# Kernel optimization log

Measured on AMD Instinct MI355X. Metric: run time of the kernel, lower is better.

The kernel has to match this reference:

```python
import jax, jax.numpy as jnp
import numpy as np

NUM_GRAPHS = 512
LEAKY_SLOPE = 0.01


def _gconv(x, src, dst, w, W_root, W_rel, b_rel):
    # PyG GraphConv: out = lin_rel(sum_j w_ij * x_j) + lin_root(x)
    msg = x[src] * w[:, None]                       # [E, d] gather + scale
    agg = jax.ops.segment_sum(msg, dst, num_segments=x.shape[0])  # scatter-add
    return agg @ W_rel + b_rel + x @ W_root


def setup_inputs() -> dict:
    key = jax.random.key(0)
    ks = jax.random.split(key, 12)
    N, E, D, H, C = 100000, 1250000, 64, 64, 8
    x_embeddings = jax.random.normal(ks[0], (N, D), dtype=jnp.float32)
    edge_index = jax.random.randint(ks[1], (2, E), 0, N, dtype=jnp.int64)
    weights = jax.random.uniform(ks[2], (E,), dtype=jnp.float32)
    batch = jnp.sort(jax.random.randint(ks[3], (N,), 0, NUM_GRAPHS, dtype=jnp.int64))
    s1 = 1.0 / np.sqrt(D)
    s2 = 1.0 / np.sqrt(H)
    W1_root = jax.random.uniform(ks[4], (D, H), jnp.float32, -s1, s1)
    W1_rel = jax.random.uniform(ks[5], (D, H), jnp.float32, -s1, s1)
    b1 = jax.random.uniform(ks[6], (H,), jnp.float32, -s1, s1)
    W2_root = jax.random.uniform(ks[7], (H, H), jnp.float32, -s2, s2)
    W2_rel = jax.random.uniform(ks[8], (H, H), jnp.float32, -s2, s2)
    b2 = jax.random.uniform(ks[9], (H,), jnp.float32, -s2, s2)
    Wl_root = jax.random.uniform(ks[10], (H, C), jnp.float32, -s2, s2)
    bl = jax.random.uniform(ks[11], (C,), jnp.float32, -s2, s2)
    return {"x_embeddings": x_embeddings, "edge_index": edge_index,
            "weights": weights, "batch": batch,
            "W1_root": W1_root, "W1_rel": W1_rel, "b1": b1,
            "W2_root": W2_root, "W2_rel": W2_rel, "b2": b2,
            "Wl_root": Wl_root, "bl": bl}


def reference(x_embeddings, edge_index, weights, batch,
              W1_root, W1_rel, b1, W2_root, W2_rel, b2, Wl_root, bl):
    src, dst = edge_index[0], edge_index[1]
    x = _gconv(x_embeddings, src, dst, weights, W1_root, W1_rel, b1)
    x = jax.nn.leaky_relu(x, LEAKY_SLOPE)
    x = _gconv(x, src, dst, weights, W2_root, W2_rel, b2)
    x = jax.nn.leaky_relu(x, LEAKY_SLOPE)
    # global_mean_pool over graph ids
    summed = jax.ops.segment_sum(x, batch, num_segments=NUM_GRAPHS)
    counts = jax.ops.segment_sum(jnp.ones((x.shape[0],), x.dtype), batch,
                                 num_segments=NUM_GRAPHS)
    pooled = summed / jnp.maximum(counts, 1.0)[:, None]
    # final GraphConv applied with no edges: agg = 0 -> W_root x + b_rel
    out = pooled @ Wl_root + bl
    return out
```

## Files before the change

kernel.cpp:

```cpp
#include <hip/hip_runtime.h>

#define LEAKY_SLOPE 0.01f
#define NUM_GRAPHS 512
#define TILE 4096
#define NB_MAX 512
#define POOL_SPAN 8

typedef __attribute__((ext_vector_type(8))) short short8;
typedef __attribute__((ext_vector_type(4))) float f32x4;

static __device__ __forceinline__ unsigned short f2bf(float f) {
    unsigned u = __float_as_uint(f);
    u += 0x7FFFu + ((u >> 16) & 1u);
    return (unsigned short)(u >> 16);
}
static __device__ __forceinline__ float bf2f(unsigned short h) {
    return __uint_as_float(((unsigned)h) << 16);
}

static __device__ __forceinline__ int wave_incl_scan(int v, int lane) {
#pragma unroll
    for (int off = 1; off < 64; off <<= 1) {
        int t = __shfl_up(v, off, 64);
        if (lane >= off) v += t;
    }
    return v;
}

__global__ __launch_bounds__(256)
void mega_prep(const int* __restrict__ dst, int* __restrict__ bucketCnt, int E,
               int NB, int histBlocks,
               const float* __restrict__ x, unsigned short* __restrict__ xB,
               int xElems , int xBlocks,
               const float* __restrict__ W1rel, const float* __restrict__ W1root,
               const float* __restrict__ W2rel, const float* __restrict__ W2root,
               unsigned short* __restrict__ Bt1, unsigned short* __restrict__ Bt2) {
    const int bid = blockIdx.x;
    if (bid < histBlocks) {
        __shared__ int h[NB_MAX];
        for (int t = threadIdx.x; t < NB_MAX; t += 256) h[t] = 0;
        __syncthreads();
        const int base = bid * TILE;
#pragma unroll
        for (int i = 0; i < TILE / 256; ++i) {
            int e = base + i * 256 + threadIdx.x;
            if (e < E) atomicAdd(&h[dst[e] >> 8], 1);
        }
        __syncthreads();
        for (int t = threadIdx.x; t < NB; t += 256)
            if (h[t]) atomicAdd(&bucketCnt[t], h[t]);
    } else if (bid < histBlocks + xBlocks) {
        int i = (bid - histBlocks) * 256 + threadIdx.x;
        if (i < xElems) {
            float4 f = ((const float4*)x)[i];
            ushort4 o = make_ushort4(f2bf(f.x), f2bf(f.y), f2bf(f.z), f2bf(f.w));
            ((ushort4*)xB)[i] = o;
        }
    } else {
        int b2 = bid - histBlocks - xBlocks;
        for (int idx = b2 * 2048 + threadIdx.x; idx < (b2 + 1) * 2048; idx += 256) {
            int which = idx >> 13;
            int j = idx & 8191;
            int n = j >> 7, k = j & 127;
            const float* Wr = which ? W2rel : W1rel;
            const float* Wo = which ? W2root : W1root;
            float v = (k < 64) ? Wr[k * 64 + n] : Wo[(k - 64) * 64 + n];
            (which ? Bt2 : Bt1)[j] = f2bf(v);
        }
    }
}

__global__ __launch_bounds__(512)
void bscan_kernel(const int* __restrict__ bucketCnt, int* __restrict__ bucketBase,
                  int* __restrict__ cursor, int* __restrict__ rowStart,
                  float* __restrict__ pooled, int N, int E, int NB) {
    __shared__ int ws[8];
    const int t = threadIdx.x, lane = t & 63, wid = t >> 6;
    int v = (t < NB) ? bucketCnt[t] : 0;
    int s = wave_incl_scan(v, lane);
    if (lane == 63) ws[wid] = s;
    __syncthreads();
    int add = 0;
    for (int i = 0; i < wid; ++i) add += ws[i];
    if (t < NB) {
        int excl = s + add - v;
        bucketBase[t] = excl;
        cursor[t] = excl;
    }
    if (t == 0) rowStart[N] = E;
    float4 z = make_float4(0.f, 0.f, 0.f, 0.f);
#pragma unroll
    for (int i = 0; i < 16; ++i)
        ((float4*)pooled)[t * 16 + i] = z;
}

__global__ __launch_bounds__(256)
void p1b_partition(const int* __restrict__ src, const int* __restrict__ dst,
                   const float* __restrict__ w, int* __restrict__ cursor,
                   int2* __restrict__ tmp, int E, int NB) {
    __shared__ int h[NB_MAX];
    __shared__ int cur[NB_MAX];
    __shared__ int lstart[NB_MAX];
    __shared__ int gbase[NB_MAX];
    __shared__ int ws[4];
    __shared__ int2 pay[TILE];
    __shared__ unsigned short bk[TILE];

    for (int t = threadIdx.x; t < NB_MAX; t += 256) h[t] = 0;
    __syncthreads();

    const int base = blockIdx.x * TILE;
    int   myb[TILE / 256];
    int   myp[TILE / 256];
    float myw[TILE / 256];
#pragma unroll
    for (int i = 0; i < TILE / 256; ++i) {
        int e = base + i * 256 + threadIdx.x;
        if (e < E) {
            int d = dst[e];
            myb[i] = d >> 8;
            myp[i] = src[e] | ((d & 255) << 20);
            myw[i] = w[e];
            atomicAdd(&h[myb[i]], 1);
        } else {
            myb[i] = -1;
        }
    }
    __syncthreads();

    {
        const int t = threadIdx.x, lane = t & 63, wid = t >> 6;
        int a = h[2 * t], b = h[2 * t + 1];
        int s = wave_incl_scan(a + b, lane);
        if (lane == 63) ws[wid] = s;
        __syncthreads();
        int add = 0;
        for (int i = 0; i < wid; ++i) add += ws[i];
        int excl = s + add - (a + b);
        lstart[2 * t] = excl;
        lstart[2 * t + 1] = excl + a;
        cur[2 * t] = excl;
        cur[2 * t + 1] = excl + a;
    }
    __syncthreads();

#pragma unroll
    for (int i = 0; i < TILE / 256; ++i) {
        if (myb[i] >= 0) {
            int p = atomicAdd(&cur[myb[i]], 1);
            pay[p] = make_int2(myp[i], __float_as_int(myw[i]));
            bk[p] = (unsigned short)myb[i];
        }
    }
    __syncthreads();

    for (int t = threadIdx.x; t < NB; t += 256) {
        int c = h[t];
        if (c) gbase[t] = atomicAdd(&cursor[t], c);
    }
    __syncthreads();

    const int total = min(TILE, E - base);
    for (int s2 = threadIdx.x; s2 < total; s2 += 256) {
        int b2 = bk[s2];
        tmp[gbase[b2] + s2 - lstart[b2]] = pay[s2];
    }
}

__global__ __launch_bounds__(256)
void p2_build(const int2* __restrict__ tmp, const int* __restrict__ bucketBase,
              int* __restrict__ rowStart, int2* __restrict__ edata,
              int N, int E, int NB) {
    const int b = blockIdx.x;
    const int s = bucketBase[b];
    const int e2 = (b + 1 < NB) ? bucketBase[b + 1] : E;
    __shared__ int h[256];
    __shared__ int cur[256];
    __shared__ int ws[4];
    h[threadIdx.x] = 0;
    __syncthreads();
    for (int j = s + threadIdx.x; j < e2; j += 256) {
        int dl = (tmp[j].x >> 20) & 255;
        atomicAdd(&h[dl], 1);
    }
    __syncthreads();
    const int t = threadIdx.x, lane = t & 63, wid = t >> 6;
    int v = h[t];
    int sc = wave_incl_scan(v, lane);
    if (lane == 63) ws[wid] = sc;
    __syncthreads();
    int add = 0;
    for (int i = 0; i < wid; ++i) add += ws[i];
    int excl = sc + add - v;
    const int node = b * 256 + t;
    if (node < N) rowStart[node] = s + excl;
    cur[t] = excl;
    __syncthreads();
    for (int j = s + threadIdx.x; j < e2; j += 256) {
        int2 v2 = tmp[j];
        int dl = (v2.x >> 20) & 255;
        int p = atomicAdd(&cur[dl], 1);
        edata[s + p] = make_int2(v2.x & 0x1FFFF, v2.y);
    }
}

template <int POOL>
__global__ __launch_bounds__(256)
void fused_layer(const unsigned short* __restrict__ xin,
                 const int* __restrict__ rowStart,
                 const int2* __restrict__ edata,
                 const unsigned short* __restrict__ Bt,
                 const float* __restrict__ bias,
                 unsigned short* __restrict__ xoutB,
                 const int* __restrict__ batch,
                 float* __restrict__ pooled, int N) {
    const int lane = threadIdx.x & 63;
    const int wave = threadIdx.x >> 6;
    const int grp  = lane >> 4;
    const int l16  = lane & 15;
    const int f4   = l16 * 4;
    const int m0   = (int)blockIdx.x * 32;

    __shared__ __align__(16) unsigned short aggL[32][72];
    __shared__ float lpool[POOL_SPAN * 64];

    int gmin = 0;
    if (POOL) {
        gmin = batch[m0 < N ? m0 : N - 1];
        for (int i = threadIdx.x; i < POOL_SPAN * 64; i += 256) lpool[i] = 0.f;
    }

    int rsv = 0;
    if (lane <= 32) {
        int rn = m0 + lane;
        rsv = rowStart[rn < N ? rn : N];
    }
#pragma unroll 1
    for (int k = 0; k < 8; ++k) {
        const int i = wave * 8 + k;
        const int s = __shfl(rsv, i, 64);
        const int e = __shfl(rsv, i + 1, 64);
        float a0 = 0.f, a1 = 0.f, a2 = 0.f, a3 = 0.f;
        for (int j = s; j < e; j += 16) {
            int2 ed[4];
#pragma unroll
            for (int u = 0; u < 4; ++u) {
                int ii = j + u * 4 + grp;
                ed[u] = edata[ii < e ? ii : s];
            }
            ushort4 r[4];
#pragma unroll
            for (int u = 0; u < 4; ++u)
                r[u] = *(const ushort4*)(xin + (size_t)ed[u].x * 64 + f4);
#pragma unroll
            for (int u = 0; u < 4; ++u) {
                float wv = (j + u * 4 + grp < e) ? __int_as_float(ed[u].y) : 0.0f;
                a0 += bf2f(r[u].x) * wv;  a1 += bf2f(r[u].y) * wv;
                a2 += bf2f(r[u].z) * wv;  a3 += bf2f(r[u].w) * wv;
            }
        }
        a0 += __shfl_xor(a0, 16, 64);  a1 += __shfl_xor(a1, 16, 64);
        a2 += __shfl_xor(a2, 16, 64);  a3 += __shfl_xor(a3, 16, 64);
        a0 += __shfl_xor(a0, 32, 64);  a1 += __shfl_xor(a1, 32, 64);
        a2 += __shfl_xor(a2, 32, 64);  a3 += __shfl_xor(a3, 32, 64);
        if (grp == 0)
            *(ushort4*)(&aggL[i][f4]) =
                make_ushort4(f2bf(a0), f2bf(a1), f2bf(a2), f2bf(a3));
    }

    __syncthreads();

    if (wave < 2) {
        const int s = wave;
        short8 bf[4][4];
#pragma unroll
        for (int t = 0; t < 4; ++t)
#pragma unroll
            for (int k = 0; k < 4; ++k)
                bf[t][k] = *(const short8*)(Bt + (t * 16 + l16) * 128 + k * 32 + grp * 8);

        f32x4 acc[4];
#pragma unroll
        for (int t = 0; t < 4; ++t)
            acc[t] = (f32x4){0.f, 0.f, 0.f, 0.f};

        {
            int row = m0 + s * 16 + l16;
            int rowc = row < N ? row : N - 1;
            const unsigned short* xrow = xin + (size_t)rowc * 64;
            short8 af[4];
            af[0] = *(const short8*)(&aggL[s * 16 + l16][grp * 8]);
            af[1] = *(const short8*)(&aggL[s * 16 + l16][32 + grp * 8]);
            af[2] = *(const short8*)(xrow + grp * 8);
            af[3] = *(const short8*)(xrow + 32 + grp * 8);
#pragma unroll
            for (int t = 0; t < 4; ++t)
#pragma unroll
                for (int k = 0; k < 4; ++k) {
                    if (POOL == 0)
                        acc[t] = __builtin_amdgcn_mfma_f32_16x16x32_bf16(
                            bf[t][k], af[k], acc[t], 0, 0, 0);
                    else
                        acc[t] = __builtin_amdgcn_mfma_f32_16x16x32_bf16(
                            af[k], bf[t][k], acc[t], 0, 0, 0);
                }
        }

        if (POOL == 0) {
            const int node = m0 + s * 16 + l16;
            if (node < N) {
#pragma unroll
                for (int t = 0; t < 4; ++t) {
                    const float4 bb = *(const float4*)(bias + t * 16 + grp * 4);
                    float v0 = acc[t][0] + bb.x;
                    float v1 = acc[t][1] + bb.y;
                    float v2 = acc[t][2] + bb.z;
                    float v3 = acc[t][3] + bb.w;
                    v0 = (v0 > 0.f) ? v0 : LEAKY_SLOPE * v0;
                    v1 = (v1 > 0.f) ? v1 : LEAKY_SLOPE * v1;
                    v2 = (v2 > 0.f) ? v2 : LEAKY_SLOPE * v2;
                    v3 = (v3 > 0.f) ? v3 : LEAKY_SLOPE * v3;
                    ushort4 o = make_ushort4(f2bf(v0), f2bf(v1), f2bf(v2), f2bf(v3));
                    *(ushort4*)(xoutB + (size_t)node * 64 + t * 16 + grp * 4) = o;
                }
            }
        } else {
#pragma unroll
            for (int t = 0; t < 4; ++t) {
                const int col = t * 16 + l16;
                const float b = bias[col];
                const int rowbase = m0 + s * 16 + grp * 4;
                float v[4]; int g[4]; int nv = 0;
#pragma unroll
                for (int r = 0; r < 4; ++r) {
                    int row = rowbase + r;
                    if (row < N) {
                        float a = acc[t][r] + b;
                        a = (a > 0.0f) ? a : LEAKY_SLOPE * a;
                        v[nv] = a;
                        g[nv] = batch[row];
                        ++nv;
                    }
                }
                if (nv == 4 && g[0] == g[3]) {
                    int gl = g[0] - gmin;
                    float sum = v[0] + v[1] + v[2] + v[3];
                    if (gl < POOL_SPAN) atomicAdd(&lpool[gl * 64 + col], sum);
                    else                atomicAdd(&pooled[g[0] * 64 + col], sum);
                } else {
                    for (int r = 0; r < nv; ++r) {
                        int gl = g[r] - gmin;
                        if (gl < POOL_SPAN) atomicAdd(&lpool[gl * 64 + col], v[r]);
                        else                atomicAdd(&pooled[g[r] * 64 + col], v[r]);
                    }
                }
            }
        }
    }

    if (POOL) {
        __syncthreads();
        for (int i = threadIdx.x; i < POOL_SPAN * 64; i += 256) {
            float vv = lpool[i];
            if (vv != 0.0f)
                atomicAdd(&pooled[(gmin + (i >> 6)) * 64 + (i & 63)], vv);
        }
    }
}

__global__ __launch_bounds__(64)
void final_kernel(const float* __restrict__ pooled, const int* __restrict__ batch,
                  int N, const float* __restrict__ Wl, const float* __restrict__ bl,
                  float* __restrict__ out) {
    const int g = blockIdx.x;
    const int j = threadIdx.x;
    __shared__ float sp[64];
    __shared__ int scnt;
    if (j == 0) {
        int lo = 0, hi = N;
        while (lo < hi) { int mid = (lo + hi) >> 1; if (batch[mid] < g) lo = mid + 1; else hi = mid; }
        const int start = lo;
        hi = N;
        while (lo < hi) { int mid = (lo + hi) >> 1; if (batch[mid] < g + 1) lo = mid + 1; else hi = mid; }
        scnt = lo - start;
    }
    __syncthreads();
    const float c = fmaxf((float)scnt, 1.0f);
    sp[j] = pooled[g * 64 + j] / c;
    __syncthreads();
    if (j < 8) {
        float acc = bl[j];
#pragma unroll
        for (int k = 0; k < 64; ++k) acc += sp[k] * Wl[k * 8 + j];
        out[g * 8 + j] = acc;
    }
}

extern "C" void kernel_launch(void* const* d_in, const int* in_sizes, int n_in,
                              void* d_out, int out_size, void* d_ws, size_t ws_size,
                              hipStream_t stream) {
    const float* x      = (const float*)d_in[0];
    const int*   ei     = (const int*)  d_in[1];
    const float* w      = (const float*)d_in[2];
    const int*   batch  = (const int*)  d_in[3];
    const float* W1root = (const float*)d_in[4];
    const float* W1rel  = (const float*)d_in[5];
    const float* b1     = (const float*)d_in[6];
    const float* W2root = (const float*)d_in[7];
    const float* W2rel  = (const float*)d_in[8];
    const float* b2     = (const float*)d_in[9];
    const float* Wl     = (const float*)d_in[10];
    const float* bl     = (const float*)d_in[11];
    float* out = (float*)d_out;

    const int E = in_sizes[2];
    const int N = in_sizes[3];
    const int* src = ei;
    const int* dst = ei + E;
    const int NB = (N + 255) / 256;

    unsigned short* xB   = (unsigned short*)d_ws;
    unsigned short* aggB = xB   + (size_t)N * 64;
    unsigned short* x1B  = aggB + (size_t)N * 64;
    int2*  tmp      = (int2*)(x1B + (size_t)N * 64);
    int2*  edata    = tmp + E;
    unsigned short* Bt1 = (unsigned short*)(edata + E);
    unsigned short* Bt2 = Bt1 + 64 * 128;
    int*   rowStart = (int*)(Bt2 + 64 * 128);
    int*   bucketCnt  = rowStart + (N + 1);
    int*   bucketBase = bucketCnt + NB_MAX;
    int*   cursor     = bucketBase + NB_MAX;
    float* pooled   = (float*)(cursor + NB_MAX);
    (void)aggB;

    const int histBlocks = (E + TILE - 1) / TILE;
    const int xElems = N * 16;
    const int xBlocks = (xElems + 255) / 256;

    (void)hipMemsetAsync(bucketCnt, 0, NB_MAX * sizeof(int), stream);
    mega_prep<<<histBlocks + xBlocks + 8, 256, 0, stream>>>(
        dst, bucketCnt, E, NB, histBlocks,
        x, xB, xElems, xBlocks,
        W1rel, W1root, W2rel, W2root, Bt1, Bt2);
    bscan_kernel<<<1, 512, 0, stream>>>(bucketCnt, bucketBase, cursor, rowStart,
                                        pooled, N, E, NB);
    p1b_partition<<<histBlocks, 256, 0, stream>>>(src, dst, w, cursor, tmp, E, NB);
    p2_build<<<NB, 256, 0, stream>>>(tmp, bucketBase, rowStart, edata, N, E, NB);

    const int fBlocks = (N + 31) / 32;
    fused_layer<0><<<fBlocks, 256, 0, stream>>>(xB, rowStart, edata, Bt1, b1,
                                                x1B, nullptr, nullptr, N);
    fused_layer<1><<<fBlocks, 256, 0, stream>>>(x1B, rowStart, edata, Bt2, b2,
                                                nullptr, batch, pooled, N);
    final_kernel<<<NUM_GRAPHS, 64, 0, stream>>>(pooled, batch, N, Wl, bl, out);
}
```

Measured before the change: 271.2 us.

## Balance edge aggregation across lanes by splitting block edge range evenly

Instead of each wave walking 8 destination rows with 4 edges per group, each 16-lane quarter-wave now takes an equal slice of the block's 32-row edge range. Local destination indices are packed into the high bits of the edge source word, and partial sums are flushed into an fp32 shared accumulator with LDS atomics whenever the destination changes. The aim is to remove load imbalance from uneven degrees and the cross-group shuffle reductions. In exchange it adds LDS atomics, an extra init pass and barrier, and a float-to-bf16 conversion before the MFMA stage.

```diff
diff --git a/kernel.cpp b/kernel.cpp
--- a/kernel.cpp
+++ b/kernel.cpp
@@ -200,7 +200,7 @@
         int2 v2 = tmp[j];
         int dl = (v2.x >> 20) & 255;
         int p = atomicAdd(&cur[dl], 1);
-        edata[s + p] = make_int2(v2.x & 0x1FFFF, v2.y);
+        edata[s + p] = make_int2((v2.x & 0x1FFFF) | (dl << 24), v2.y);
     }
 }
 
@@ -219,53 +219,65 @@
     const int grp  = lane >> 4;
     const int l16  = lane & 15;
     const int f4   = l16 * 4;
+    const int qq   = threadIdx.x >> 4;
     const int m0   = (int)blockIdx.x * 32;
 
-    __shared__ __align__(16) unsigned short aggL[32][72];
+    __shared__ __align__(16) float aggLf[32][68];
     __shared__ float lpool[POOL_SPAN * 64];
 
+    for (int i = threadIdx.x; i < 32 * 68; i += 256) ((float*)aggLf)[i] = 0.f;
     int gmin = 0;
     if (POOL) {
         gmin = batch[m0 < N ? m0 : N - 1];
         for (int i = threadIdx.x; i < POOL_SPAN * 64; i += 256) lpool[i] = 0.f;
     }
-
-    int rsv = 0;
-    if (lane <= 32) {
-        int rn = m0 + lane;
-        rsv = rowStart[rn < N ? rn : N];
-    }
-#pragma unroll 1
-    for (int k = 0; k < 8; ++k) {
-        const int i = wave * 8 + k;
-        const int s = __shfl(rsv, i, 64);
-        const int e = __shfl(rsv, i + 1, 64);
+    const int S  = rowStart[m0 < N ? m0 : N];
+    const int E2 = rowStart[(m0 + 32) < N ? (m0 + 32) : N];
+    __syncthreads();
+
+    {
+        const int base8 = m0 & 255;
+        const int qlen = E2 - S;
+        const int qs = S + ((qlen * qq) >> 4);
+        const int qe = S + ((qlen * (qq + 1)) >> 4);
+
         float a0 = 0.f, a1 = 0.f, a2 = 0.f, a3 = 0.f;
-        for (int j = s; j < e; j += 16) {
+        int dcur = -1;
+        for (int j = qs; j < qe; j += 4) {
             int2 ed[4];
+            ushort4 r[4];
 #pragma unroll
             for (int u = 0; u < 4; ++u) {
-                int ii = j + u * 4 + grp;
-                ed[u] = edata[ii < e ? ii : s];
+                int ii = j + u;
+                ed[u] = edata[ii < qe ? ii : qe - 1];
             }
-            ushort4 r[4];
 #pragma unroll
             for (int u = 0; u < 4; ++u)
-                r[u] = *(const ushort4*)(xin + (size_t)ed[u].x * 64 + f4);
+                r[u] = *(const ushort4*)(xin + (size_t)(ed[u].x & 0xFFFFFF) * 64 + f4);
 #pragma unroll
             for (int u = 0; u < 4; ++u) {
-                float wv = (j + u * 4 + grp < e) ? __int_as_float(ed[u].y) : 0.0f;
+                int dl = (int)((unsigned)ed[u].x >> 24) - base8;
+                if (dl != dcur) {
+                    if (dcur >= 0) {
+                        atomicAdd(&aggLf[dcur][f4 + 0], a0);
+                        atomicAdd(&aggLf[dcur][f4 + 1], a1);
+                        atomicAdd(&aggLf[dcur][f4 + 2], a2);
+                        atomicAdd(&aggLf[dcur][f4 + 3], a3);
+                    }
+                    a0 = a1 = a2 = a3 = 0.f;
+                    dcur = dl;
+                }
+                float wv = (j + u < qe) ? __int_as_float(ed[u].y) : 0.0f;
                 a0 += bf2f(r[u].x) * wv;  a1 += bf2f(r[u].y) * wv;
                 a2 += bf2f(r[u].z) * wv;  a3 += bf2f(r[u].w) * wv;
             }
         }
-        a0 += __shfl_xor(a0, 16, 64);  a1 += __shfl_xor(a1, 16, 64);
-        a2 += __shfl_xor(a2, 16, 64);  a3 += __shfl_xor(a3, 16, 64);
-        a0 += __shfl_xor(a0, 32, 64);  a1 += __shfl_xor(a1, 32, 64);
-        a2 += __shfl_xor(a2, 32, 64);  a3 += __shfl_xor(a3, 32, 64);
-        if (grp == 0)
-            *(ushort4*)(&aggL[i][f4]) =
-                make_ushort4(f2bf(a0), f2bf(a1), f2bf(a2), f2bf(a3));
+        if (dcur >= 0) {
+            atomicAdd(&aggLf[dcur][f4 + 0], a0);
+            atomicAdd(&aggLf[dcur][f4 + 1], a1);
+            atomicAdd(&aggLf[dcur][f4 + 2], a2);
+            atomicAdd(&aggLf[dcur][f4 + 3], a3);
+        }
     }
 
     __syncthreads();
@@ -288,9 +300,20 @@
             int row = m0 + s * 16 + l16;
             int rowc = row < N ? row : N - 1;
             const unsigned short* xrow = xin + (size_t)rowc * 64;
+            const float* arow = aggLf[s * 16 + l16];
+            float4 q0 = *(const float4*)(arow + grp * 8);
+            float4 q1 = *(const float4*)(arow + grp * 8 + 4);
+            float4 q2 = *(const float4*)(arow + 32 + grp * 8);
+            float4 q3 = *(const float4*)(arow + 32 + grp * 8 + 4);
             short8 af[4];
-            af[0] = *(const short8*)(&aggL[s * 16 + l16][grp * 8]);
-            af[1] = *(const short8*)(&aggL[s * 16 + l16][32 + grp * 8]);
+            af[0][0] = (short)f2bf(q0.x); af[0][1] = (short)f2bf(q0.y);
+            af[0][2] = (short)f2bf(q0.z); af[0][3] = (short)f2bf(q0.w);
+            af[0][4] = (short)f2bf(q1.x); af[0][5] = (short)f2bf(q1.y);
+            af[0][6] = (short)f2bf(q1.z); af[0][7] = (short)f2bf(q1.w);
+            af[1][0] = (short)f2bf(q2.x); af[1][1] = (short)f2bf(q2.y);
+            af[1][2] = (short)f2bf(q2.z); af[1][3] = (short)f2bf(q2.w);
+            af[1][4] = (short)f2bf(q3.x); af[1][5] = (short)f2bf(q3.y);
+            af[1][6] = (short)f2bf(q3.z); af[1][7] = (short)f2bf(q3.w);
             af[2] = *(const short8*)(xrow + grp * 8);
             af[3] = *(const short8*)(xrow + 32 + grp * 8);
 #pragma unroll
```

Result: slower. 290.4 us (+7.1%).

## Use 512-thread blocks with two interleaved row gathers per wave and all-wave MFMA

Applied to the files above, without the earlier changes.

The fused layer kernel now runs 8 waves per block instead of 4. Each wave aggregates 4 rows as two pairs, and within each pair it walks both rows' edge lists together, so more independent gather loads are in flight at once. The MFMA stage is split so all 8 waves each compute one 16x16 output tile, where before only 2 waves each computed 4 tiles. The aim is more memory-level parallelism and better use of the waves in the matmul/epilogue. The cost is extra branching and register pressure in the interleaved loop, plus larger blocks that may lower occupancy.

```diff
diff --git a/kernel.cpp b/kernel.cpp
--- a/kernel.cpp
+++ b/kernel.cpp
@@ -205,7 +205,7 @@
 }
 
 template <int POOL>
-__global__ __launch_bounds__(256)
+__global__ __launch_bounds__(512)
 void fused_layer(const unsigned short* __restrict__ xin,
                  const int* __restrict__ rowStart,
                  const int2* __restrict__ edata,
@@ -227,7 +227,7 @@
     int gmin = 0;
     if (POOL) {
         gmin = batch[m0 < N ? m0 : N - 1];
-        for (int i = threadIdx.x; i < POOL_SPAN * 64; i += 256) lpool[i] = 0.f;
+        for (int i = threadIdx.x; i < POOL_SPAN * 64; i += 512) lpool[i] = 0.f;
     }
 
     int rsv = 0;
@@ -235,124 +235,149 @@
         int rn = m0 + lane;
         rsv = rowStart[rn < N ? rn : N];
     }
-#pragma unroll 1
-    for (int k = 0; k < 8; ++k) {
-        const int i = wave * 8 + k;
-        const int s = __shfl(rsv, i, 64);
-        const int e = __shfl(rsv, i + 1, 64);
-        float a0 = 0.f, a1 = 0.f, a2 = 0.f, a3 = 0.f;
-        for (int j = s; j < e; j += 16) {
-            int2 ed[4];
-#pragma unroll
-            for (int u = 0; u < 4; ++u) {
-                int ii = j + u * 4 + grp;
-                ed[u] = edata[ii < e ? ii : s];
-            }
-            ushort4 r[4];
-#pragma unroll
-            for (int u = 0; u < 4; ++u)
-                r[u] = *(const ushort4*)(xin + (size_t)ed[u].x * 64 + f4);
-#pragma unroll
-            for (int u = 0; u < 4; ++u) {
-                float wv = (j + u * 4 + grp < e) ? __int_as_float(ed[u].y) : 0.0f;
-                a0 += bf2f(r[u].x) * wv;  a1 += bf2f(r[u].y) * wv;
-                a2 += bf2f(r[u].z) * wv;  a3 += bf2f(r[u].w) * wv;
-            }
-        }
-        a0 += __shfl_xor(a0, 16, 64);  a1 += __shfl_xor(a1, 16, 64);
-        a2 += __shfl_xor(a2, 16, 64);  a3 += __shfl_xor(a3, 16, 64);
-        a0 += __shfl_xor(a0, 32, 64);  a1 += __shfl_xor(a1, 32, 64);
-        a2 += __shfl_xor(a2, 32, 64);  a3 += __shfl_xor(a3, 32, 64);
-        if (grp == 0)
-            *(ushort4*)(&aggL[i][f4]) =
-                make_ushort4(f2bf(a0), f2bf(a1), f2bf(a2), f2bf(a3));
-    }
-
-    __syncthreads();
-
-    if (wave < 2) {
-        const int s = wave;
-        short8 bf[4][4];
-#pragma unroll
-        for (int t = 0; t < 4; ++t)
-#pragma unroll
-            for (int k = 0; k < 4; ++k)
-                bf[t][k] = *(const short8*)(Bt + (t * 16 + l16) * 128 + k * 32 + grp * 8);
-
-        f32x4 acc[4];
-#pragma unroll
-        for (int t = 0; t < 4; ++t)
-            acc[t] = (f32x4){0.f, 0.f, 0.f, 0.f};
-
-        {
-            int row = m0 + s * 16 + l16;
-            int rowc = row < N ? row : N - 1;
-            const unsigned short* xrow = xin + (size_t)rowc * 64;
-            short8 af[4];
-            af[0] = *(const short8*)(&aggL[s * 16 + l16][grp * 8]);
-            af[1] = *(const short8*)(&aggL[s * 16 + l16][32 + grp * 8]);
-            af[2] = *(const short8*)(xrow + grp * 8);
-            af[3] = *(const short8*)(xrow + 32 + grp * 8);
-#pragma unroll
-            for (int t = 0; t < 4; ++t)
-#pragma unroll
-                for (int k = 0; k < 4; ++k) {
-                    if (POOL == 0)
-                        acc[t] = __builtin_amdgcn_mfma_f32_16x16x32_bf16(
-                            bf[t][k], af[k], acc[t], 0, 0, 0);
-                    else
-                        acc[t] = __builtin_amdgcn_mfma_f32_16x16x32_bf16(
-                            af[k], bf[t][k], acc[t], 0, 0, 0);
-                }
+#pragma unroll
+    for (int p = 0; p < 2; ++p) {
+        const int ia = (wave << 2) + (p << 1);
+        const int sa = __shfl(rsv, ia, 64);
+        const int ea = __shfl(rsv, ia + 1, 64);
+        const int sb = ea;
+        const int eb = __shfl(rsv, ia + 2, 64);
+
+        float aA0 = 0.f, aA1 = 0.f, aA2 = 0.f, aA3 = 0.f;
+        float aB0 = 0.f, aB1 = 0.f, aB2 = 0.f, aB3 = 0.f;
+        int ja = sa, jb = sb;
+        while (ja < ea || jb < eb) {
+            const bool da = ja < ea;
+            const bool db = jb < eb;
+            int2 edA[4], edB[4];
+            if (da) {
+#pragma unroll
+                for (int u = 0; u < 4; ++u) {
+                    int ii = ja + u * 4 + grp;
+                    edA[u] = edata[ii < ea ? ii : sa];
+                }
+            }
+            if (db) {
+#pragma unroll
+                for (int u = 0; u < 4; ++u) {
+                    int ii = jb + u * 4 + grp;
+                    edB[u] = edata[ii < eb ? ii : sb];
+                }
+            }
+            ushort4 rA[4], rB[4];
+            if (da) {
+#pragma unroll
+                for (int u = 0; u < 4; ++u)
+                    rA[u] = *(const ushort4*)(xin + (size_t)edA[u].x * 64 + f4);
+            }
+            if (db) {
+#pragma unroll
+                for (int u = 0; u < 4; ++u)
+                    rB[u] = *(const ushort4*)(xin + (size_t)edB[u].x * 64 + f4);
+            }
+            if (da) {
+#pragma unroll
+                for (int u = 0; u < 4; ++u) {
+                    float wv = (ja + u * 4 + grp < ea) ? __int_as_float(edA[u].y) : 0.0f;
+                    aA0 += bf2f(rA[u].x) * wv;  aA1 += bf2f(rA[u].y) * wv;
+                    aA2 += bf2f(rA[u].z) * wv;  aA3 += bf2f(rA[u].w) * wv;
+                }
+                ja += 16;
+            }
+            if (db) {
+#pragma unroll
+                for (int u = 0; u < 4; ++u) {
+                    float wv = (jb + u * 4 + grp < eb) ? __int_as_float(edB[u].y) : 0.0f;
+                    aB0 += bf2f(rB[u].x) * wv;  aB1 += bf2f(rB[u].y) * wv;
+                    aB2 += bf2f(rB[u].z) * wv;  aB3 += bf2f(rB[u].w) * wv;
+                }
+                jb += 16;
+            }
+        }
+        aA0 += __shfl_xor(aA0, 16, 64);  aA1 += __shfl_xor(aA1, 16, 64);
+        aA2 += __shfl_xor(aA2, 16, 64);  aA3 += __shfl_xor(aA3, 16, 64);
+        aA0 += __shfl_xor(aA0, 32, 64);  aA1 += __shfl_xor(aA1, 32, 64);
+        aA2 += __shfl_xor(aA2, 32, 64);  aA3 += __shfl_xor(aA3, 32, 64);
+        aB0 += __shfl_xor(aB0, 16, 64);  aB1 += __shfl_xor(aB1, 16, 64);
+        aB2 += __shfl_xor(aB2, 16, 64);  aB3 += __shfl_xor(aB3, 16, 64);
+        aB0 += __shfl_xor(aB0, 32, 64);  aB1 += __shfl_xor(aB1, 32, 64);
+        aB2 += __shfl_xor(aB2, 32, 64);  aB3 += __shfl_xor(aB3, 32, 64);
+        if (grp == 0) {
+            *(ushort4*)(&aggL[ia][f4]) =
+                make_ushort4(f2bf(aA0), f2bf(aA1), f2bf(aA2), f2bf(aA3));
+            *(ushort4*)(&aggL[ia + 1][f4]) =
+                make_ushort4(f2bf(aB0), f2bf(aB1), f2bf(aB2), f2bf(aB3));
+        }
+    }
+
+    __syncthreads();
+
+    {
+        const int s = wave >> 2;
+        const int t = wave & 3;
+        short8 bf[4];
+#pragma unroll
+        for (int k = 0; k < 4; ++k)
+            bf[k] = *(const short8*)(Bt + (t * 16 + l16) * 128 + k * 32 + grp * 8);
+
+        f32x4 acc = (f32x4){0.f, 0.f, 0.f, 0.f};
+        int row = m0 + s * 16 + l16;
+        int rowc = row < N ? row : N - 1;
+        const unsigned short* xrow = xin + (size_t)rowc * 64;
+        short8 af[4];
+        af[0] = *(const short8*)(&aggL[s * 16 + l16][grp * 8]);
+        af[1] = *(const short8*)(&aggL[s * 16 + l16][32 + grp * 8]);
+        af[2] = *(const short8*)(xrow + grp * 8);
+        af[3] = *(const short8*)(xrow + 32 + grp * 8);
+#pragma unroll
+        for (int k = 0; k < 4; ++k) {
+            if (POOL == 0)
+                acc = __builtin_amdgcn_mfma_f32_16x16x32_bf16(bf[k], af[k], acc, 0, 0, 0);
+            else
+                acc = __builtin_amdgcn_mfma_f32_16x16x32_bf16(af[k], bf[k], acc, 0, 0, 0);
         }
 
         if (POOL == 0) {
             const int node = m0 + s * 16 + l16;
             if (node < N) {
-#pragma unroll
-                for (int t = 0; t < 4; ++t) {
-                    const float4 bb = *(const float4*)(bias + t * 16 + grp * 4);
-                    float v0 = acc[t][0] + bb.x;
-                    float v1 = acc[t][1] + bb.y;
-                    float v2 = acc[t][2] + bb.z;
-                    float v3 = acc[t][3] + bb.w;
-                    v0 = (v0 > 0.f) ? v0 : LEAKY_SLOPE * v0;
-                    v1 = (v1 > 0.f) ? v1 : LEAKY_SLOPE * v1;
-                    v2 = (v2 > 0.f) ? v2 : LEAKY_SLOPE * v2;
-                    v3 = (v3 > 0.f) ? v3 : LEAKY_SLOPE * v3;
-                    ushort4 o = make_ushort4(f2bf(v0), f2bf(v1), f2bf(v2), f2bf(v3));
-                    *(ushort4*)(xoutB + (size_t)node * 64 + t * 16 + grp * 4) = o;
-                }
+                const float4 bb = *(const float4*)(bias + t * 16 + grp * 4);
+                float v0 = acc[0] + bb.x;
+                float v1 = acc[1] + bb.y;
+                float v2 = acc[2] + bb.z;
+                float v3 = acc[3] + bb.w;
+                v0 = (v0 > 0.f) ? v0 : LEAKY_SLOPE * v0;
+                v1 = (v1 > 0.f) ? v1 : LEAKY_SLOPE * v1;
+                v2 = (v2 > 0.f) ? v2 : LEAKY_SLOPE * v2;
+                v3 = (v3 > 0.f) ? v3 : LEAKY_SLOPE * v3;
+                ushort4 o = make_ushort4(f2bf(v0), f2bf(v1), f2bf(v2), f2bf(v3));
+                *(ushort4*)(xoutB + (size_t)node * 64 + t * 16 + grp * 4) = o;
             }
         } else {
-#pragma unroll
-            for (int t = 0; t < 4; ++t) {
-                const int col = t * 16 + l16;
-                const float b = bias[col];
-                const int rowbase = m0 + s * 16 + grp * 4;
-                float v[4]; int g[4]; int nv = 0;
-#pragma unroll
-                for (int r = 0; r < 4; ++r) {
-                    int row = rowbase + r;
-                    if (row < N) {
-                        float a = acc[t][r] + b;
-                        a = (a > 0.0f) ? a : LEAKY_SLOPE * a;
-                        v[nv] = a;
-                        g[nv] = batch[row];
-                        ++nv;
-                    }
-                }
-                if (nv == 4 && g[0] == g[3]) {
-                    int gl = g[0] - gmin;
-                    float sum = v[0] + v[1] + v[2] + v[3];
-                    if (gl < POOL_SPAN) atomicAdd(&lpool[gl * 64 + col], sum);
-                    else                atomicAdd(&pooled[g[0] * 64 + col], sum);
-                } else {
-                    for (int r = 0; r < nv; ++r) {
-                        int gl = g[r] - gmin;
-                        if (gl < POOL_SPAN) atomicAdd(&lpool[gl * 64 + col], v[r]);
-                        else                atomicAdd(&pooled[g[r] * 64 + col], v[r]);
-                    }
+            const int col = t * 16 + l16;
+            const float b = bias[col];
+            const int rowbase = m0 + s * 16 + grp * 4;
+            float v[4]; int g[4]; int nv = 0;
+#pragma unroll
+            for (int r = 0; r < 4; ++r) {
+                int row2 = rowbase + r;
+                if (row2 < N) {
+                    float a = acc[r] + b;
+                    a = (a > 0.0f) ? a : LEAKY_SLOPE * a;
+                    v[nv] = a;
+                    g[nv] = batch[row2];
+                    ++nv;
+                }
+            }
+            if (nv == 4 && g[0] == g[3]) {
+                int gl = g[0] - gmin;
+                float sum = v[0] + v[1] + v[2] + v[3];
+                if (gl < POOL_SPAN) atomicAdd(&lpool[gl * 64 + col], sum);
+                else                atomicAdd(&pooled[g[0] * 64 + col], sum);
+            } else {
+                for (int r = 0; r < nv; ++r) {
+                    int gl = g[r] - gmin;
+                    if (gl < POOL_SPAN) atomicAdd(&lpool[gl * 64 + col], v[r]);
+                    else                atomicAdd(&pooled[g[r] * 64 + col], v[r]);
                 }
             }
         }
@@ -360,7 +385,7 @@
 
     if (POOL) {
         __syncthreads();
-        for (int i = threadIdx.x; i < POOL_SPAN * 64; i += 256) {
+        for (int i = threadIdx.x; i < POOL_SPAN * 64; i += 512) {
             float vv = lpool[i];
             if (vv != 0.0f)
                 atomicAdd(&pooled[(gmin + (i >> 6)) * 64 + (i & 63)], vv);
@@ -448,9 +473,9 @@
     p2_build<<<NB, 256, 0, stream>>>(tmp, bucketBase, rowStart, edata, N, E, NB);
 
     const int fBlocks = (N + 31) / 32;
-    fused_layer<0><<<fBlocks, 256, 0, stream>>>(xB, rowStart, edata, Bt1, b1,
+    fused_layer<0><<<fBlocks, 512, 0, stream>>>(xB, rowStart, edata, Bt1, b1,
                                                 x1B, nullptr, nullptr, N);
-    fused_layer<1><<<fBlocks, 256, 0, stream>>>(x1B, rowStart, edata, Bt2, b2,
+    fused_layer<1><<<fBlocks, 512, 0, stream>>>(x1B, rowStart, edata, Bt2, b2,
                                                 nullptr, batch, pooled, N);
     final_kernel<<<NUM_GRAPHS, 64, 0, stream>>>(pooled, batch, N, Wl, bl, out);
 }
```

After: 280.2 us. +3.3%, slower.
